# Performance work log

Measured on AMD Instinct MI355X. Metric: run time of the kernel, lower is better.

## Reference

```python
import jax, jax.numpy as jnp
import numpy as np

N_NODES = 50000
N_EDGES = 600000
D = 128


def setup_inputs() -> dict:
    key = jax.random.key(0)
    ks = jax.random.split(key, 8)
    s = 0.05
    return {
        "x": jax.random.normal(ks[0], (N_NODES, D), jnp.float32),
        "edge_index": jax.random.randint(ks[1], (2, N_EDGES), 0, N_NODES, jnp.int64),
        "edge_attr": jax.random.normal(ks[2], (N_EDGES, D), jnp.float32),
        "We1": jax.random.normal(ks[3], (3 * D, D), jnp.float32) * s,
        "be1": jnp.zeros((D,), jnp.float32),
        "We2": jax.random.normal(ks[4], (D, D), jnp.float32) * s,
        "be2": jnp.zeros((D,), jnp.float32),
        "Wn1": jax.random.normal(ks[5], (2 * D, D), jnp.float32) * s,
        "bn1": jnp.zeros((D,), jnp.float32),
        "Wn2": jax.random.normal(ks[6], (D, D), jnp.float32) * s,
        "bn2": jnp.zeros((D,), jnp.float32),
    }


def reference(x, edge_index, edge_attr, We1, be1, We2, be2, Wn1, bn1, Wn2, bn2):
    src = edge_index[0]
    dest = edge_index[1]
    n = x.shape[0]
    # edge model: MLP on [x_src | x_dest | edge_attr]  -> [E, D]
    e_in = jnp.concatenate([x[src], x[dest], edge_attr], axis=-1)
    e = jax.nn.relu(e_in @ We1 + be1) @ We2 + be2
    # node model: scatter-mean of updated edge_attr into dest nodes
    agg = jax.ops.segment_sum(e, dest, num_segments=n)
    cnt = jax.ops.segment_sum(jnp.ones((e.shape[0],), e.dtype), dest, num_segments=n)
    agg = agg / jnp.maximum(cnt, 1.0)[:, None]
    n_in = jnp.concatenate([x, agg], axis=-1)
    x_out = jax.nn.relu(n_in @ Wn1 + bn1) @ Wn2 + bn2
    return x_out, e
```

## Files before the change

kernel.cpp:

```cpp
#include <hip/hip_runtime.h>
#include <hip/hip_bf16.h>

#define DD 128

typedef short bf16x8 __attribute__((ext_vector_type(8)));
typedef float f32x4 __attribute__((ext_vector_type(4)));

__device__ __forceinline__ unsigned short f2b(float f) {
  unsigned int u = __float_as_uint(f);
  u = u + 0x7FFFu + ((u >> 16) & 1u);
  return (unsigned short)(u >> 16);
}

#define GLDS16(gp, lp) __builtin_amdgcn_global_load_lds( \
    (const __attribute__((address_space(1))) unsigned int*)(const void*)(gp), \
    (__attribute__((address_space(3))) unsigned int*)(void*)(lp), 16, 0, 0)

__global__ __launch_bounds__(256) void cvt_x_kernel(const float* __restrict__ x,
                                                    unsigned short* __restrict__ xb, int n4) {
  const int i = blockIdx.x * 256 + threadIdx.x;
  if (i < n4) {
    const float4 v = reinterpret_cast<const float4*>(x)[i];
    ushort4 o;
    o.x = f2b(v.x); o.y = f2b(v.y); o.z = f2b(v.z); o.w = f2b(v.w);
    reinterpret_cast<ushort4*>(xb)[i] = o;
  }
}

__global__ void count_kernel(const int* __restrict__ ei, int* __restrict__ cnt, int E) {
  int i = blockIdx.x * blockDim.x + threadIdx.x;
  if (i < E) atomicAdd(&cnt[ei[E + i]], 1);
}

__global__ __launch_bounds__(256) void scan_a(const int* __restrict__ cnt,
                                              int* __restrict__ off,
                                              int* __restrict__ bsum, int N) {
  __shared__ int wsum[4];
  const int t = threadIdx.x;
  const int i0 = blockIdx.x * 1024 + t * 4;
  int4 v = {0, 0, 0, 0};
  if (i0 + 3 < N) v = *reinterpret_cast<const int4*>(cnt + i0);
  else {
    if (i0 < N)     v.x = cnt[i0];
    if (i0 + 1 < N) v.y = cnt[i0 + 1];
    if (i0 + 2 < N) v.z = cnt[i0 + 2];
    if (i0 + 3 < N) v.w = cnt[i0 + 3];
  }
  const int s1 = v.x, s2 = s1 + v.y, s3 = s2 + v.z, tot = s3 + v.w;
  const int lane = t & 63, wv = t >> 6;
  int sc = tot;
#pragma unroll
  for (int d = 1; d < 64; d <<= 1) {
    int u = __shfl_up(sc, d);
    if (lane >= d) sc += u;
  }
  if (lane == 63) wsum[wv] = sc;
  __syncthreads();
  int wpre = 0;
  for (int w = 0; w < wv; ++w) wpre += wsum[w];
  const int excl = wpre + sc - tot;
  if (i0 < N)     off[i0]     = excl;
  if (i0 + 1 < N) off[i0 + 1] = excl + s1;
  if (i0 + 2 < N) off[i0 + 2] = excl + s2;
  if (i0 + 3 < N) off[i0 + 3] = excl + s3;
  if (t == 255) bsum[blockIdx.x] = wpre + sc;
}

__global__ void scan_b(int* __restrict__ bsum, int B) {
  const int t = threadIdx.x;
  const int v0 = (t < B) ? bsum[t] : 0;
  int v = v0;
#pragma unroll
  for (int d = 1; d < 64; d <<= 1) {
    int u = __shfl_up(v, d);
    if (t >= d) v += u;
  }
  if (t < B) bsum[t] = v - v0;
}

__global__ __launch_bounds__(256) void scan_c(int* __restrict__ off, int* __restrict__ cur,
                                              const int* __restrict__ bsum, int N, int E) {
  const int t = threadIdx.x;
  const int add = bsum[blockIdx.x];
  const int i0 = blockIdx.x * 1024 + t * 4;
#pragma unroll
  for (int k = 0; k < 4; ++k) {
    const int i = i0 + k;
    if (i < N) {
      const int o = off[i] + add;
      off[i] = o;
      cur[i] = o;
    }
  }
  if (blockIdx.x == 0 && t == 0) off[N] = E;
}

__global__ void fill_kernel(const int* __restrict__ ei, int* __restrict__ cur,
                            int* __restrict__ perm, int E) {
  int i = blockIdx.x * blockDim.x + threadIdx.x;
  if (i < E) {
    const int d = ei[E + i];
    const int pos = atomicAdd(&cur[d], 1);
    perm[pos] = i;
  }
}

__global__ __launch_bounds__(256, 2) void edge_mlp_kernel(
    const unsigned short* __restrict__ xb,
    const int* __restrict__ ei,
    const float* __restrict__ ea,
    const float* __restrict__ We1,
    const float* __restrict__ be1,
    const float* __restrict__ We2,
    const float* __restrict__ be2,
    float* __restrict__ e_out,
    int E)
{
  __shared__ __align__(16) unsigned short xs_lds[64][128];
  __shared__ __align__(16) unsigned short xd_lds[64][128];
  __shared__ __align__(16) unsigned short ea_lds[64][128];
  __shared__ __align__(16) unsigned short h_lds[64][136];
  __shared__ int srcs[64], dsts[64];

  const int tid  = threadIdx.x;
  const int wv   = tid >> 6;
  const int lane = tid & 63;
  const int lg   = lane >> 4;
  const int lm   = lane & 15;

  bf16x8 w1f[12][2];
  bf16x8 w2f[4][2];
  float b1[2], b2[2];
#pragma unroll
  for (int nf = 0; nf < 2; ++nf) {
    const int n = wv * 32 + nf * 16 + lm;
    b1[nf] = be1[n];
    b2[nf] = be2[n];
#pragma unroll
    for (int kb = 0; kb < 12; ++kb) {
      bf16x8 f;
#pragma unroll
      for (int j = 0; j < 8; ++j)
        f[j] = (short)f2b(We1[(kb * 32 + lg * 8 + j) * DD + n]);
      w1f[kb][nf] = f;
    }
#pragma unroll
    for (int kb = 0; kb < 4; ++kb) {
      bf16x8 f;
#pragma unroll
      for (int j = 0; j < 8; ++j)
        f[j] = (short)f2b(We2[(kb * 32 + lg * 8 + j) * DD + n]);
      w2f[kb][nf] = f;
    }
  }

  const int ntiles = E >> 6;
  for (int tile = blockIdx.x; tile < ntiles; tile += gridDim.x) {
    const int ebase = tile << 6;
    __syncthreads();

    if (tid < 64)       srcs[tid]      = ei[ebase + tid];
    else if (tid < 128) dsts[tid - 64] = ei[E + ebase + tid - 64];
    __syncthreads();

    {
#pragma unroll
      for (int wl = 0; wl < 4; ++wl) {
        const int r0 = wv * 16 + wl * 4;
        const int r  = r0 + (lane >> 4);
        const int ch = (lane & 15) ^ (r & 7);
        GLDS16(xb + (size_t)srcs[r] * DD + ch * 8, &xs_lds[r0][0]);
        GLDS16(xb + (size_t)dsts[r] * DD + ch * 8, &xd_lds[r0][0]);
      }
    }

    {
      float4 va[4], vb[4];
#pragma unroll
      for (int it = 0; it < 4; ++it) {
        const int q = tid + it * 256;
        const int r = q >> 4;
        const int c = q & 15;
        const float* p = ea + (size_t)(ebase + r) * DD + c * 8;
        va[it] = *reinterpret_cast<const float4*>(p);
        vb[it] = *reinterpret_cast<const float4*>(p + 4);
      }
#pragma unroll
      for (int it = 0; it < 4; ++it) {
        const int q = tid + it * 256;
        const int r = q >> 4;
        const int c = q & 15;
        bf16x8 o;
        o[0] = (short)f2b(va[it].x); o[1] = (short)f2b(va[it].y);
        o[2] = (short)f2b(va[it].z); o[3] = (short)f2b(va[it].w);
        o[4] = (short)f2b(vb[it].x); o[5] = (short)f2b(vb[it].y);
        o[6] = (short)f2b(vb[it].z); o[7] = (short)f2b(vb[it].w);
        *reinterpret_cast<bf16x8*>(&ea_lds[r][(c ^ (r & 7)) * 8]) = o;
      }
    }
    __syncthreads();

    f32x4 acc[4][2];
#pragma unroll
    for (int mf = 0; mf < 4; ++mf)
#pragma unroll
      for (int nf = 0; nf < 2; ++nf)
        acc[mf][nf] = (f32x4){0.f, 0.f, 0.f, 0.f};

#pragma unroll
    for (int kb = 0; kb < 12; ++kb) {
      const unsigned short (*blk)[128] = (kb < 4) ? xs_lds : (kb < 8) ? xd_lds : ea_lds;
      const int kl = kb & 3;
      bf16x8 a[4];
#pragma unroll
      for (int mf = 0; mf < 4; ++mf) {
        const int r = mf * 16 + lm;
        a[mf] = *reinterpret_cast<const bf16x8*>(&blk[r][((kl * 4 + lg) ^ (r & 7)) * 8]);
      }
#pragma unroll
      for (int mf = 0; mf < 4; ++mf)
#pragma unroll
        for (int nf = 0; nf < 2; ++nf)
          acc[mf][nf] = __builtin_amdgcn_mfma_f32_16x16x32_bf16(a[mf], w1f[kb][nf], acc[mf][nf], 0, 0, 0);
    }

#pragma unroll
    for (int mf = 0; mf < 4; ++mf)
#pragma unroll
      for (int nf = 0; nf < 2; ++nf)
#pragma unroll
        for (int rg = 0; rg < 4; ++rg) {
          const int m = mf * 16 + lg * 4 + rg;
          const int n = wv * 32 + nf * 16 + lm;
          float v = acc[mf][nf][rg] + b1[nf];
          h_lds[m][n] = f2b(v > 0.f ? v : 0.f);
        }
    __syncthreads();

    f32x4 acc2[4][2];
#pragma unroll
    for (int mf = 0; mf < 4; ++mf)
#pragma unroll
      for (int nf = 0; nf < 2; ++nf)
        acc2[mf][nf] = (f32x4){0.f, 0.f, 0.f, 0.f};

#pragma unroll
    for (int kb = 0; kb < 4; ++kb) {
      bf16x8 a[4];
#pragma unroll
      for (int mf = 0; mf < 4; ++mf)
        a[mf] = *reinterpret_cast<const bf16x8*>(&h_lds[mf * 16 + lm][kb * 32 + lg * 8]);
#pragma unroll
      for (int mf = 0; mf < 4; ++mf)
#pragma unroll
        for (int nf = 0; nf < 2; ++nf)
          acc2[mf][nf] = __builtin_amdgcn_mfma_f32_16x16x32_bf16(a[mf], w2f[kb][nf], acc2[mf][nf], 0, 0, 0);
    }

#pragma unroll
    for (int mf = 0; mf < 4; ++mf)
#pragma unroll
      for (int rg = 0; rg < 4; ++rg) {
        const int gm = ebase + mf * 16 + lg * 4 + rg;
#pragma unroll
        for (int nf = 0; nf < 2; ++nf) {
          const int n = wv * 32 + nf * 16 + lm;
          e_out[(size_t)gm * DD + n] = acc2[mf][nf][rg] + b2[nf];
        }
      }
  }
}

__global__ __launch_bounds__(256) void agg_kernel(const float* __restrict__ e_out,
                                                  const int* __restrict__ off,
                                                  const int* __restrict__ perm,
                                                  float* __restrict__ agg, int N) {
  const int wv   = threadIdx.x >> 6;
  const int lane = threadIdx.x & 63;
  const int nid  = blockIdx.x * 4 + wv;
  if (nid >= N) return;
  const int o0 = off[nid], o1 = off[nid + 1];
  float2 s0 = {0.f, 0.f}, s1 = {0.f, 0.f}, s2 = {0.f, 0.f}, s3 = {0.f, 0.f};
  int j = o0;
  for (; j + 4 <= o1; j += 4) {
    const int r0 = perm[j], r1 = perm[j + 1], r2 = perm[j + 2], r3 = perm[j + 3];
    const float2 v0 = *reinterpret_cast<const float2*>(e_out + (size_t)r0 * DD + (lane << 1));
    const float2 v1 = *reinterpret_cast<const float2*>(e_out + (size_t)r1 * DD + (lane << 1));
    const float2 v2 = *reinterpret_cast<const float2*>(e_out + (size_t)r2 * DD + (lane << 1));
    const float2 v3 = *reinterpret_cast<const float2*>(e_out + (size_t)r3 * DD + (lane << 1));
    s0.x += v0.x; s0.y += v0.y;
    s1.x += v1.x; s1.y += v1.y;
    s2.x += v2.x; s2.y += v2.y;
    s3.x += v3.x; s3.y += v3.y;
  }
  for (; j < o1; ++j) {
    const int r = perm[j];
    const float2 v = *reinterpret_cast<const float2*>(e_out + (size_t)r * DD + (lane << 1));
    s0.x += v.x; s0.y += v.y;
  }
  const int deg = o1 - o0;
  const float inv = deg > 0 ? 1.f / (float)deg : 0.f;
  float2 o;
  o.x = (s0.x + s1.x + s2.x + s3.x) * inv;
  o.y = (s0.y + s1.y + s2.y + s3.y) * inv;
  *reinterpret_cast<float2*>(agg + (size_t)nid * DD + (lane << 1)) = o;
}

__global__ __launch_bounds__(256, 2) void node_mlp_kernel(
    const float* __restrict__ x,
    const float* __restrict__ Wn1,
    const float* __restrict__ bn1,
    const float* __restrict__ Wn2,
    const float* __restrict__ bn2,
    float* __restrict__ xout,
    int N)
{
  __shared__ __align__(16) unsigned short A_lds[64][264];
  __shared__ __align__(16) unsigned short h_lds[64][136];

  const int tid  = threadIdx.x;
  const int wv   = tid >> 6;
  const int lane = tid & 63;
  const int lg   = lane >> 4;
  const int lm   = lane & 15;

  bf16x8 w1f[8][2];
  bf16x8 w2f[4][2];
  float b1[2], b2[2];
#pragma unroll
  for (int nf = 0; nf < 2; ++nf) {
    const int n = wv * 32 + nf * 16 + lm;
    b1[nf] = bn1[n];
    b2[nf] = bn2[n];
#pragma unroll
    for (int kb = 0; kb < 8; ++kb) {
      bf16x8 f;
#pragma unroll
      for (int j = 0; j < 8; ++j)
        f[j] = (short)f2b(Wn1[(kb * 32 + lg * 8 + j) * DD + n]);
      w1f[kb][nf] = f;
    }
#pragma unroll
    for (int kb = 0; kb < 4; ++kb) {
      bf16x8 f;
#pragma unroll
      for (int j = 0; j < 8; ++j)
        f[j] = (short)f2b(Wn2[(kb * 32 + lg * 8 + j) * DD + n]);
      w2f[kb][nf] = f;
    }
  }

  const int ntiles = (N + 63) >> 6;
  for (int tile = blockIdx.x; tile < ntiles; tile += gridDim.x) {
    const int nbase = tile << 6;
    __syncthreads();

#pragma unroll
    for (int it = 0; it < 16; ++it) {
      const int q = tid + it * 256;
      const int r = q >> 6;
      const int c = q & 63;
      int gr = nbase + r;
      if (gr >= N) gr = N - 1;
      float4 v;
      if (c < 32) v = *reinterpret_cast<const float4*>(x + (size_t)gr * DD + (c << 2));
      else        v = *reinterpret_cast<const float4*>(xout + (size_t)gr * DD + ((c - 32) << 2));
      unsigned short* dst = &A_lds[r][c << 2];
      dst[0] = f2b(v.x); dst[1] = f2b(v.y); dst[2] = f2b(v.z); dst[3] = f2b(v.w);
    }
    __syncthreads();

    f32x4 acc[4][2];
#pragma unroll
    for (int mf = 0; mf < 4; ++mf)
#pragma unroll
      for (int nf = 0; nf < 2; ++nf)
        acc[mf][nf] = (f32x4){0.f, 0.f, 0.f, 0.f};

#pragma unroll
    for (int kb = 0; kb < 8; ++kb) {
      bf16x8 a[4];
#pragma unroll
      for (int mf = 0; mf < 4; ++mf)
        a[mf] = *reinterpret_cast<const bf16x8*>(&A_lds[mf * 16 + lm][kb * 32 + lg * 8]);
#pragma unroll
      for (int mf = 0; mf < 4; ++mf)
#pragma unroll
        for (int nf = 0; nf < 2; ++nf)
          acc[mf][nf] = __builtin_amdgcn_mfma_f32_16x16x32_bf16(a[mf], w1f[kb][nf], acc[mf][nf], 0, 0, 0);
    }

#pragma unroll
    for (int mf = 0; mf < 4; ++mf)
#pragma unroll
      for (int nf = 0; nf < 2; ++nf)
#pragma unroll
        for (int rg = 0; rg < 4; ++rg) {
          const int m = mf * 16 + lg * 4 + rg;
          const int n = wv * 32 + nf * 16 + lm;
          float v = acc[mf][nf][rg] + b1[nf];
          h_lds[m][n] = f2b(v > 0.f ? v : 0.f);
        }
    __syncthreads();

    f32x4 acc2[4][2];
#pragma unroll
    for (int mf = 0; mf < 4; ++mf)
#pragma unroll
      for (int nf = 0; nf < 2; ++nf)
        acc2[mf][nf] = (f32x4){0.f, 0.f, 0.f, 0.f};

#pragma unroll
    for (int kb = 0; kb < 4; ++kb) {
      bf16x8 a[4];
#pragma unroll
      for (int mf = 0; mf < 4; ++mf)
        a[mf] = *reinterpret_cast<const bf16x8*>(&h_lds[mf * 16 + lm][kb * 32 + lg * 8]);
#pragma unroll
      for (int mf = 0; mf < 4; ++mf)
#pragma unroll
        for (int nf = 0; nf < 2; ++nf)
          acc2[mf][nf] = __builtin_amdgcn_mfma_f32_16x16x32_bf16(a[mf], w2f[kb][nf], acc2[mf][nf], 0, 0, 0);
    }

#pragma unroll
    for (int mf = 0; mf < 4; ++mf)
#pragma unroll
      for (int rg = 0; rg < 4; ++rg) {
        const int gm = nbase + mf * 16 + lg * 4 + rg;
        if (gm < N) {
#pragma unroll
          for (int nf = 0; nf < 2; ++nf) {
            const int n = wv * 32 + nf * 16 + lm;
            xout[(size_t)gm * DD + n] = acc2[mf][nf][rg] + b2[nf];
          }
        }
      }
  }
}

extern "C" void kernel_launch(void* const* d_in, const int* in_sizes, int n_in,
                              void* d_out, int out_size, void* d_ws, size_t ws_size,
                              hipStream_t stream) {
  const float* x   = (const float*)d_in[0];
  const int*   ei  = (const int*)d_in[1];
  const float* ea  = (const float*)d_in[2];
  const float* We1 = (const float*)d_in[3];
  const float* be1 = (const float*)d_in[4];
  const float* We2 = (const float*)d_in[5];
  const float* be2 = (const float*)d_in[6];
  const float* Wn1 = (const float*)d_in[7];
  const float* bn1 = (const float*)d_in[8];
  const float* Wn2 = (const float*)d_in[9];
  const float* bn2 = (const float*)d_in[10];

  const int N = in_sizes[0] / DD;
  const int E = in_sizes[2] / DD;

  float* out   = (float*)d_out;
  float* xout  = out;
  float* e_out = out + (size_t)N * DD;

  unsigned short* xb = (unsigned short*)xout;

  int* cnt  = (int*)d_ws;
  int* off  = cnt + N;
  int* cur  = off + N + 1;
  int* perm = cur + N;
  int* bsum = perm + E;

  const int SCAN_B = (N + 1023) / 1024;

  hipMemsetAsync(cnt, 0, (size_t)N * sizeof(int), stream);

  cvt_x_kernel<<<(N * DD / 4 + 255) / 256, 256, 0, stream>>>(x, xb, N * DD / 4);

  count_kernel<<<(E + 255) / 256, 256, 0, stream>>>(ei, cnt, E);
  scan_a<<<SCAN_B, 256, 0, stream>>>(cnt, off, bsum, N);
  scan_b<<<1, 64, 0, stream>>>(bsum, SCAN_B);
  scan_c<<<SCAN_B, 256, 0, stream>>>(off, cur, bsum, N, E);
  fill_kernel<<<(E + 255) / 256, 256, 0, stream>>>(ei, cur, perm, E);

  edge_mlp_kernel<<<2048, 256, 0, stream>>>(xb, ei, ea, We1, be1, We2, be2, e_out, E);

  agg_kernel<<<(N + 3) / 4, 256, 0, stream>>>(e_out, off, perm, xout, N);

  const int node_tiles = (N + 63) / 64;
  node_mlp_kernel<<<node_tiles, 256, 0, stream>>>(x, Wn1, bn1, Wn2, bn2, xout, N);
}
```

Baseline: 385.2 us.

## Fuse mean aggregation into node MLP and transpose MFMA operands for vector stores

Removes the separate agg kernel: node_mlp now gathers each node's incoming edge rows through the CSR perm and writes the bf16 mean directly into its LDS A tile, so the agg buffer no longer round-trips through global memory. Both MLP kernels swap the MFMA operand order so each lane holds four consecutive output columns. That allows float4 bias loads, float4 global stores and bf16x4 LDS writes. The hidden-layer buffer now reuses the edge-attr and A-tile LDS with XOR swizzling and an extra barrier, which cuts LDS use and raises the launch-bounds occupancy hint from 2 to 3. The risk is that the per-row serial gather inside node_mlp (16 rows per wave) may load-balance worse than the old one-wave-per-node agg kernel.

```diff
diff --git a/kernel.cpp b/kernel.cpp
--- a/kernel.cpp
+++ b/kernel.cpp
@@ -4,6 +4,7 @@
 #define DD 128
 
 typedef short bf16x8 __attribute__((ext_vector_type(8)));
+typedef short bf16x4 __attribute__((ext_vector_type(4)));
 typedef float f32x4 __attribute__((ext_vector_type(4)));
 
 __device__ __forceinline__ unsigned short f2b(float f) {
@@ -105,7 +106,7 @@
   }
 }
 
-__global__ __launch_bounds__(256, 2) void edge_mlp_kernel(
+__global__ __launch_bounds__(256, 3) void edge_mlp_kernel(
     const unsigned short* __restrict__ xb,
     const int* __restrict__ ei,
     const float* __restrict__ ea,
@@ -118,8 +119,7 @@
 {
   __shared__ __align__(16) unsigned short xs_lds[64][128];
   __shared__ __align__(16) unsigned short xd_lds[64][128];
-  __shared__ __align__(16) unsigned short ea_lds[64][128];
-  __shared__ __align__(16) unsigned short h_lds[64][136];
+  __shared__ __align__(16) unsigned short u_lds[64][128];
   __shared__ int srcs[64], dsts[64];
 
   const int tid  = threadIdx.x;
@@ -130,12 +130,12 @@
 
   bf16x8 w1f[12][2];
   bf16x8 w2f[4][2];
-  float b1[2], b2[2];
+  float4 b1v[2], b2v[2];
 #pragma unroll
   for (int nf = 0; nf < 2; ++nf) {
     const int n = wv * 32 + nf * 16 + lm;
-    b1[nf] = be1[n];
-    b2[nf] = be2[n];
+    b1v[nf] = *reinterpret_cast<const float4*>(&be1[wv * 32 + nf * 16 + 4 * lg]);
+    b2v[nf] = *reinterpret_cast<const float4*>(&be2[wv * 32 + nf * 16 + 4 * lg]);
 #pragma unroll
     for (int kb = 0; kb < 12; ++kb) {
       bf16x8 f;
@@ -163,15 +163,13 @@
     else if (tid < 128) dsts[tid - 64] = ei[E + ebase + tid - 64];
     __syncthreads();
 
-    {
-#pragma unroll
-      for (int wl = 0; wl < 4; ++wl) {
-        const int r0 = wv * 16 + wl * 4;
-        const int r  = r0 + (lane >> 4);
-        const int ch = (lane & 15) ^ (r & 7);
-        GLDS16(xb + (size_t)srcs[r] * DD + ch * 8, &xs_lds[r0][0]);
-        GLDS16(xb + (size_t)dsts[r] * DD + ch * 8, &xd_lds[r0][0]);
-      }
+#pragma unroll
+    for (int wl = 0; wl < 4; ++wl) {
+      const int r0 = wv * 16 + wl * 4;
+      const int r  = r0 + lg;
+      const int ch = lm ^ (r & 7);
+      GLDS16(xb + (size_t)srcs[r] * DD + ch * 8, &xs_lds[r0][0]);
+      GLDS16(xb + (size_t)dsts[r] * DD + ch * 8, &xd_lds[r0][0]);
     }
 
     {
@@ -179,9 +177,7 @@
 #pragma unroll
       for (int it = 0; it < 4; ++it) {
         const int q = tid + it * 256;
-        const int r = q >> 4;
-        const int c = q & 15;
-        const float* p = ea + (size_t)(ebase + r) * DD + c * 8;
+        const float* p = ea + (size_t)(ebase + (q >> 4)) * DD + (q & 15) * 8;
         va[it] = *reinterpret_cast<const float4*>(p);
         vb[it] = *reinterpret_cast<const float4*>(p + 4);
       }
@@ -195,7 +191,7 @@
         o[2] = (short)f2b(va[it].z); o[3] = (short)f2b(va[it].w);
         o[4] = (short)f2b(vb[it].x); o[5] = (short)f2b(vb[it].y);
         o[6] = (short)f2b(vb[it].z); o[7] = (short)f2b(vb[it].w);
-        *reinterpret_cast<bf16x8*>(&ea_lds[r][(c ^ (r & 7)) * 8]) = o;
+        *reinterpret_cast<bf16x8*>(&u_lds[r][(c ^ (r & 7)) * 8]) = o;
       }
     }
     __syncthreads();
@@ -209,7 +205,7 @@
 
 #pragma unroll
     for (int kb = 0; kb < 12; ++kb) {
-      const unsigned short (*blk)[128] = (kb < 4) ? xs_lds : (kb < 8) ? xd_lds : ea_lds;
+      const unsigned short (*blk)[128] = (kb < 4) ? xs_lds : (kb < 8) ? xd_lds : u_lds;
       const int kl = kb & 3;
       bf16x8 a[4];
 #pragma unroll
@@ -221,20 +217,26 @@
       for (int mf = 0; mf < 4; ++mf)
 #pragma unroll
         for (int nf = 0; nf < 2; ++nf)
-          acc[mf][nf] = __builtin_amdgcn_mfma_f32_16x16x32_bf16(a[mf], w1f[kb][nf], acc[mf][nf], 0, 0, 0);
-    }
-
-#pragma unroll
-    for (int mf = 0; mf < 4; ++mf)
-#pragma unroll
-      for (int nf = 0; nf < 2; ++nf)
+          acc[mf][nf] = __builtin_amdgcn_mfma_f32_16x16x32_bf16(w1f[kb][nf], a[mf], acc[mf][nf], 0, 0, 0);
+    }
+    __syncthreads();
+
+#pragma unroll
+    for (int mf = 0; mf < 4; ++mf) {
+      const int m = mf * 16 + lm;
+#pragma unroll
+      for (int nf = 0; nf < 2; ++nf) {
+        bf16x4 hv;
 #pragma unroll
         for (int rg = 0; rg < 4; ++rg) {
-          const int m = mf * 16 + lg * 4 + rg;
-          const int n = wv * 32 + nf * 16 + lm;
-          float v = acc[mf][nf][rg] + b1[nf];
-          h_lds[m][n] = f2b(v > 0.f ? v : 0.f);
+          float v = acc[mf][nf][rg] +
+                    (rg == 0 ? b1v[nf].x : rg == 1 ? b1v[nf].y : rg == 2 ? b1v[nf].z : b1v[nf].w);
+          hv[rg] = (short)f2b(v > 0.f ? v : 0.f);
         }
+        const int ch = (wv * 4 + nf * 2 + (lg >> 1)) ^ (m & 7);
+        *reinterpret_cast<bf16x4*>(&u_lds[m][ch * 8 + 4 * (lg & 1)]) = hv;
+      }
+    }
     __syncthreads();
 
     f32x4 acc2[4][2];
@@ -248,66 +250,38 @@
     for (int kb = 0; kb < 4; ++kb) {
       bf16x8 a[4];
 #pragma unroll
+      for (int mf = 0; mf < 4; ++mf) {
+        const int r = mf * 16 + lm;
+        a[mf] = *reinterpret_cast<const bf16x8*>(&u_lds[r][((kb * 4 + lg) ^ (r & 7)) * 8]);
+      }
+#pragma unroll
       for (int mf = 0; mf < 4; ++mf)
-        a[mf] = *reinterpret_cast<const bf16x8*>(&h_lds[mf * 16 + lm][kb * 32 + lg * 8]);
-#pragma unroll
-      for (int mf = 0; mf < 4; ++mf)
 #pragma unroll
         for (int nf = 0; nf < 2; ++nf)
-          acc2[mf][nf] = __builtin_amdgcn_mfma_f32_16x16x32_bf16(a[mf], w2f[kb][nf], acc2[mf][nf], 0, 0, 0);
-    }
-
-#pragma unroll
-    for (int mf = 0; mf < 4; ++mf)
-#pragma unroll
-      for (int rg = 0; rg < 4; ++rg) {
-        const int gm = ebase + mf * 16 + lg * 4 + rg;
-#pragma unroll
-        for (int nf = 0; nf < 2; ++nf) {
-          const int n = wv * 32 + nf * 16 + lm;
-          e_out[(size_t)gm * DD + n] = acc2[mf][nf][rg] + b2[nf];
-        }
-      }
-  }
-}
-
-__global__ __launch_bounds__(256) void agg_kernel(const float* __restrict__ e_out,
-                                                  const int* __restrict__ off,
-                                                  const int* __restrict__ perm,
-                                                  float* __restrict__ agg, int N) {
-  const int wv   = threadIdx.x >> 6;
-  const int lane = threadIdx.x & 63;
-  const int nid  = blockIdx.x * 4 + wv;
-  if (nid >= N) return;
-  const int o0 = off[nid], o1 = off[nid + 1];
-  float2 s0 = {0.f, 0.f}, s1 = {0.f, 0.f}, s2 = {0.f, 0.f}, s3 = {0.f, 0.f};
-  int j = o0;
-  for (; j + 4 <= o1; j += 4) {
-    const int r0 = perm[j], r1 = perm[j + 1], r2 = perm[j + 2], r3 = perm[j + 3];
-    const float2 v0 = *reinterpret_cast<const float2*>(e_out + (size_t)r0 * DD + (lane << 1));
-    const float2 v1 = *reinterpret_cast<const float2*>(e_out + (size_t)r1 * DD + (lane << 1));
-    const float2 v2 = *reinterpret_cast<const float2*>(e_out + (size_t)r2 * DD + (lane << 1));
-    const float2 v3 = *reinterpret_cast<const float2*>(e_out + (size_t)r3 * DD + (lane << 1));
-    s0.x += v0.x; s0.y += v0.y;
-    s1.x += v1.x; s1.y += v1.y;
-    s2.x += v2.x; s2.y += v2.y;
-    s3.x += v3.x; s3.y += v3.y;
-  }
-  for (; j < o1; ++j) {
-    const int r = perm[j];
-    const float2 v = *reinterpret_cast<const float2*>(e_out + (size_t)r * DD + (lane << 1));
-    s0.x += v.x; s0.y += v.y;
-  }
-  const int deg = o1 - o0;
-  const float inv = deg > 0 ? 1.f / (float)deg : 0.f;
-  float2 o;
-  o.x = (s0.x + s1.x + s2.x + s3.x) * inv;
-  o.y = (s0.y + s1.y + s2.y + s3.y) * inv;
-  *reinterpret_cast<float2*>(agg + (size_t)nid * DD + (lane << 1)) = o;
-}
-
-__global__ __launch_bounds__(256, 2) void node_mlp_kernel(
+          acc2[mf][nf] = __builtin_amdgcn_mfma_f32_16x16x32_bf16(w2f[kb][nf], a[mf], acc2[mf][nf], 0, 0, 0);
+    }
+
+#pragma unroll
+    for (int mf = 0; mf < 4; ++mf) {
+      const int gm = ebase + mf * 16 + lm;
+#pragma unroll
+      for (int nf = 0; nf < 2; ++nf) {
+        float4 o;
+        o.x = acc2[mf][nf][0] + b2v[nf].x;
+        o.y = acc2[mf][nf][1] + b2v[nf].y;
+        o.z = acc2[mf][nf][2] + b2v[nf].z;
+        o.w = acc2[mf][nf][3] + b2v[nf].w;
+        *reinterpret_cast<float4*>(&e_out[(size_t)gm * DD + wv * 32 + nf * 16 + 4 * lg]) = o;
+      }
+    }
+  }
+}
+
+__global__ __launch_bounds__(256, 3) void node_mlp_kernel(
     const float* __restrict__ x,
+    const float* __restrict__ e_out,
+    const int* __restrict__ off,
+    const int* __restrict__ perm,
     const float* __restrict__ Wn1,
     const float* __restrict__ bn1,
     const float* __restrict__ Wn2,
@@ -315,8 +289,7 @@
     float* __restrict__ xout,
     int N)
 {
-  __shared__ __align__(16) unsigned short A_lds[64][264];
-  __shared__ __align__(16) unsigned short h_lds[64][136];
+  __shared__ __align__(16) unsigned short A_lds[64 * 256];
 
   const int tid  = threadIdx.x;
   const int wv   = tid >> 6;
@@ -326,12 +299,12 @@
 
   bf16x8 w1f[8][2];
   bf16x8 w2f[4][2];
-  float b1[2], b2[2];
+  float4 b1v[2], b2v[2];
 #pragma unroll
   for (int nf = 0; nf < 2; ++nf) {
     const int n = wv * 32 + nf * 16 + lm;
-    b1[nf] = bn1[n];
-    b2[nf] = bn2[n];
+    b1v[nf] = *reinterpret_cast<const float4*>(&bn1[wv * 32 + nf * 16 + 4 * lg]);
+    b2v[nf] = *reinterpret_cast<const float4*>(&bn2[wv * 32 + nf * 16 + 4 * lg]);
 #pragma unroll
     for (int kb = 0; kb < 8; ++kb) {
       bf16x8 f;
@@ -356,17 +329,47 @@
     __syncthreads();
 
 #pragma unroll
-    for (int it = 0; it < 16; ++it) {
+    for (int it = 0; it < 4; ++it) {
       const int q = tid + it * 256;
-      const int r = q >> 6;
-      const int c = q & 63;
-      int gr = nbase + r;
-      if (gr >= N) gr = N - 1;
-      float4 v;
-      if (c < 32) v = *reinterpret_cast<const float4*>(x + (size_t)gr * DD + (c << 2));
-      else        v = *reinterpret_cast<const float4*>(xout + (size_t)gr * DD + ((c - 32) << 2));
-      unsigned short* dst = &A_lds[r][c << 2];
-      dst[0] = f2b(v.x); dst[1] = f2b(v.y); dst[2] = f2b(v.z); dst[3] = f2b(v.w);
+      const int r = q >> 4;
+      const int c = q & 15;
+      int gr = nbase + r; if (gr >= N) gr = N - 1;
+      const float* p = x + (size_t)gr * DD + c * 8;
+      const float4 va = *reinterpret_cast<const float4*>(p);
+      const float4 vb = *reinterpret_cast<const float4*>(p + 4);
+      bf16x8 o;
+      o[0] = (short)f2b(va.x); o[1] = (short)f2b(va.y);
+      o[2] = (short)f2b(va.z); o[3] = (short)f2b(va.w);
+      o[4] = (short)f2b(vb.x); o[5] = (short)f2b(vb.y);
+      o[6] = (short)f2b(vb.z); o[7] = (short)f2b(vb.w);
+      *reinterpret_cast<bf16x8*>(&A_lds[r * 256 + ((c ^ (r & 7)) * 8)]) = o;
+    }
+
+    for (int rr = 0; rr < 16; ++rr) {
+      const int row = wv * 16 + rr;
+      int gr = nbase + row; if (gr >= N) gr = N - 1;
+      const int o0 = off[gr], o1 = off[gr + 1];
+      float sx0 = 0.f, sy0 = 0.f, sx1 = 0.f, sy1 = 0.f;
+      int j = o0;
+      for (; j + 2 <= o1; j += 2) {
+        const int p0 = perm[j], p1 = perm[j + 1];
+        const float2 v0 = *reinterpret_cast<const float2*>(e_out + (size_t)p0 * DD + 2 * lane);
+        const float2 v1 = *reinterpret_cast<const float2*>(e_out + (size_t)p1 * DD + 2 * lane);
+        sx0 += v0.x; sy0 += v0.y;
+        sx1 += v1.x; sy1 += v1.y;
+      }
+      if (j < o1) {
+        const int p0 = perm[j];
+        const float2 v0 = *reinterpret_cast<const float2*>(e_out + (size_t)p0 * DD + 2 * lane);
+        sx0 += v0.x; sy0 += v0.y;
+      }
+      const int deg = o1 - o0;
+      const float inv = deg > 0 ? 1.f / (float)deg : 0.f;
+      const unsigned int pk = (unsigned int)f2b((sx0 + sx1) * inv) |
+                              ((unsigned int)f2b((sy0 + sy1) * inv) << 16);
+      const int cA = 16 + (lane >> 2);
+      *reinterpret_cast<unsigned int*>(
+          &A_lds[row * 256 + ((cA ^ (row & 7)) * 8) + 2 * (lane & 3)]) = pk;
     }
     __syncthreads();
 
@@ -381,26 +384,35 @@
     for (int kb = 0; kb < 8; ++kb) {
       bf16x8 a[4];
 #pragma unroll
+      for (int mf = 0; mf < 4; ++mf) {
+        const int r = mf * 16 + lm;
+        a[mf] = *reinterpret_cast<const bf16x8*>(
+            &A_lds[r * 256 + (((kb * 4 + lg) ^ (r & 7)) * 8)]);
+      }
+#pragma unroll
       for (int mf = 0; mf < 4; ++mf)
-        a[mf] = *reinterpret_cast<const bf16x8*>(&A_lds[mf * 16 + lm][kb * 32 + lg * 8]);
-#pragma unroll
-      for (int mf = 0; mf < 4; ++mf)
 #pragma unroll
         for (int nf = 0; nf < 2; ++nf)
-          acc[mf][nf] = __builtin_amdgcn_mfma_f32_16x16x32_bf16(a[mf], w1f[kb][nf], acc[mf][nf], 0, 0, 0);
-    }
-
-#pragma unroll
-    for (int mf = 0; mf < 4; ++mf)
-#pragma unroll
-      for (int nf = 0; nf < 2; ++nf)
+          acc[mf][nf] = __builtin_amdgcn_mfma_f32_16x16x32_bf16(w1f[kb][nf], a[mf], acc[mf][nf], 0, 0, 0);
+    }
+    __syncthreads();
+
+#pragma unroll
+    for (int mf = 0; mf < 4; ++mf) {
+      const int m = mf * 16 + lm;
+#pragma unroll
+      for (int nf = 0; nf < 2; ++nf) {
+        bf16x4 hv;
 #pragma unroll
         for (int rg = 0; rg < 4; ++rg) {
-          const int m = mf * 16 + lg * 4 + rg;
-          const int n = wv * 32 + nf * 16 + lm;
-          float v = acc[mf][nf][rg] + b1[nf];
-          h_lds[m][n] = f2b(v > 0.f ? v : 0.f);
+          float v = acc[mf][nf][rg] +
+                    (rg == 0 ? b1v[nf].x : rg == 1 ? b1v[nf].y : rg == 2 ? b1v[nf].z : b1v[nf].w);
+          hv[rg] = (short)f2b(v > 0.f ? v : 0.f);
         }
+        const int ch = (wv * 4 + nf * 2 + (lg >> 1)) ^ (m & 7);
+        *reinterpret_cast<bf16x4*>(&A_lds[m * 128 + ch * 8 + 4 * (lg & 1)]) = hv;
+      }
+    }
     __syncthreads();
 
     f32x4 acc2[4][2];
@@ -414,28 +426,33 @@
     for (int kb = 0; kb < 4; ++kb) {
       bf16x8 a[4];
 #pragma unroll
+      for (int mf = 0; mf < 4; ++mf) {
+        const int r = mf * 16 + lm;
+        a[mf] = *reinterpret_cast<const bf16x8*>(
+            &A_lds[r * 128 + (((kb * 4 + lg) ^ (r & 7)) * 8)]);
+      }
+#pragma unroll
       for (int mf = 0; mf < 4; ++mf)
-        a[mf] = *reinterpret_cast<const bf16x8*>(&h_lds[mf * 16 + lm][kb * 32 + lg * 8]);
-#pragma unroll
-      for (int mf = 0; mf < 4; ++mf)
 #pragma unroll
         for (int nf = 0; nf < 2; ++nf)
-          acc2[mf][nf] = __builtin_amdgcn_mfma_f32_16x16x32_bf16(a[mf], w2f[kb][nf], acc2[mf][nf], 0, 0, 0);
-    }
-
-#pragma unroll
-    for (int mf = 0; mf < 4; ++mf)
-#pragma unroll
-      for (int rg = 0; rg < 4; ++rg) {
-        const int gm = nbase + mf * 16 + lg * 4 + rg;
-        if (gm < N) {
-#pragma unroll
-          for (int nf = 0; nf < 2; ++nf) {
-            const int n = wv * 32 + nf * 16 + lm;
-            xout[(size_t)gm * DD + n] = acc2[mf][nf][rg] + b2[nf];
-          }
+          acc2[mf][nf] = __builtin_amdgcn_mfma_f32_16x16x32_bf16(w2f[kb][nf], a[mf], acc2[mf][nf], 0, 0, 0);
+    }
+
+#pragma unroll
+    for (int mf = 0; mf < 4; ++mf) {
+      const int gm = nbase + mf * 16 + lm;
+      if (gm < N) {
+#pragma unroll
+        for (int nf = 0; nf < 2; ++nf) {
+          float4 o;
+          o.x = acc2[mf][nf][0] + b2v[nf].x;
+          o.y = acc2[mf][nf][1] + b2v[nf].y;
+          o.z = acc2[mf][nf][2] + b2v[nf].z;
+          o.w = acc2[mf][nf][3] + b2v[nf].w;
+          *reinterpret_cast<float4*>(&xout[(size_t)gm * DD + wv * 32 + nf * 16 + 4 * lg]) = o;
         }
       }
+    }
   }
 }
 
@@ -483,8 +500,7 @@
 
   edge_mlp_kernel<<<2048, 256, 0, stream>>>(xb, ei, ea, We1, be1, We2, be2, e_out, E);
 
-  agg_kernel<<<(N + 3) / 4, 256, 0, stream>>>(e_out, off, perm, xout, N);
-
   const int node_tiles = (N + 63) / 64;
-  node_mlp_kernel<<<node_tiles, 256, 0, stream>>>(x, Wn1, bn1, Wn2, bn2, xout, N);
-}
+  node_mlp_kernel<<<node_tiles, 256, 0, stream>>>(x, e_out, off, perm,
+                                                  Wn1, bn1, Wn2, bn2, xout, N);
+}
```

Result: slower. 619.8 us (+60.9%).

## Precompute per-node src/dest projections of We1 and gather them per edge

Applied to the files above, without the earlier changes.

Splits the first edge-layer GEMM by linearity: a new kernel computes x@We1[0:128] and x@We1[128:256] once per node into a bf16 buffer. The edge kernel then gathers these per-edge projections as the accumulator initialisation and only runs the edge_attr third of the K dimension. This removes two thirds of the edge-layer MFMA work and the gathered x tiles from LDS, which lowers LDS use and allows higher occupancy. In exchange, the per-edge gather becomes scalar bf16 loads of 256-wide rows, and the projections are rounded to bf16 before summation.

```diff
diff --git a/kernel.cpp b/kernel.cpp
--- a/kernel.cpp
+++ b/kernel.cpp
@@ -11,20 +11,8 @@
   u = u + 0x7FFFu + ((u >> 16) & 1u);
   return (unsigned short)(u >> 16);
 }
-
-#define GLDS16(gp, lp) __builtin_amdgcn_global_load_lds( \
-    (const __attribute__((address_space(1))) unsigned int*)(const void*)(gp), \
-    (__attribute__((address_space(3))) unsigned int*)(void*)(lp), 16, 0, 0)
-
-__global__ __launch_bounds__(256) void cvt_x_kernel(const float* __restrict__ x,
-                                                    unsigned short* __restrict__ xb, int n4) {
-  const int i = blockIdx.x * 256 + threadIdx.x;
-  if (i < n4) {
-    const float4 v = reinterpret_cast<const float4*>(x)[i];
-    ushort4 o;
-    o.x = f2b(v.x); o.y = f2b(v.y); o.z = f2b(v.z); o.w = f2b(v.w);
-    reinterpret_cast<ushort4*>(xb)[i] = o;
-  }
+__device__ __forceinline__ float b2f(unsigned short u) {
+  return __uint_as_float((unsigned int)u << 16);
 }
 
 __global__ void count_kernel(const int* __restrict__ ei, int* __restrict__ cnt, int E) {
@@ -105,8 +93,93 @@
   }
 }
 
-__global__ __launch_bounds__(256, 2) void edge_mlp_kernel(
-    const unsigned short* __restrict__ xb,
+__global__ __launch_bounds__(256, 2) void pq_kernel(
+    const float* __restrict__ x,
+    const float* __restrict__ We1,
+    unsigned short* __restrict__ pq,
+    int N)
+{
+  __shared__ __align__(16) unsigned short x_lds[64][128];
+
+  const int tid  = threadIdx.x;
+  const int wv   = tid >> 6;
+  const int lane = tid & 63;
+  const int lg   = lane >> 4;
+  const int lm   = lane & 15;
+
+  bf16x8 wf[4][4];
+#pragma unroll
+  for (int nf = 0; nf < 4; ++nf) {
+    const int n    = wv * 64 + nf * 16 + lm;
+    const int col  = n & 127;
+    const int kro  = (n >> 7) * 128;
+#pragma unroll
+    for (int kb = 0; kb < 4; ++kb) {
+      bf16x8 f;
+#pragma unroll
+      for (int j = 0; j < 8; ++j)
+        f[j] = (short)f2b(We1[(kro + kb * 32 + lg * 8 + j) * DD + col]);
+      wf[kb][nf] = f;
+    }
+  }
+
+  const int nbase = blockIdx.x * 64;
+
+#pragma unroll
+  for (int it = 0; it < 4; ++it) {
+    const int q = tid + it * 256;
+    const int r = q >> 4;
+    const int c = q & 15;
+    int gr = nbase + r; if (gr >= N) gr = N - 1;
+    const float* p = x + (size_t)gr * DD + c * 8;
+    const float4 va = *reinterpret_cast<const float4*>(p);
+    const float4 vb = *reinterpret_cast<const float4*>(p + 4);
+    bf16x8 o;
+    o[0] = (short)f2b(va.x); o[1] = (short)f2b(va.y);
+    o[2] = (short)f2b(va.z); o[3] = (short)f2b(va.w);
+    o[4] = (short)f2b(vb.x); o[5] = (short)f2b(vb.y);
+    o[6] = (short)f2b(vb.z); o[7] = (short)f2b(vb.w);
+    *reinterpret_cast<bf16x8*>(&x_lds[r][(c ^ (r & 7)) * 8]) = o;
+  }
+  __syncthreads();
+
+  f32x4 acc[4][4];
+#pragma unroll
+  for (int mf = 0; mf < 4; ++mf)
+#pragma unroll
+    for (int nf = 0; nf < 4; ++nf)
+      acc[mf][nf] = (f32x4){0.f, 0.f, 0.f, 0.f};
+
+#pragma unroll
+  for (int kb = 0; kb < 4; ++kb) {
+    bf16x8 a[4];
+#pragma unroll
+    for (int mf = 0; mf < 4; ++mf) {
+      const int r = mf * 16 + lm;
+      a[mf] = *reinterpret_cast<const bf16x8*>(&x_lds[r][((kb * 4 + lg) ^ (r & 7)) * 8]);
+    }
+#pragma unroll
+    for (int mf = 0; mf < 4; ++mf)
+#pragma unroll
+      for (int nf = 0; nf < 4; ++nf)
+        acc[mf][nf] = __builtin_amdgcn_mfma_f32_16x16x32_bf16(a[mf], wf[kb][nf], acc[mf][nf], 0, 0, 0);
+  }
+
+#pragma unroll
+  for (int mf = 0; mf < 4; ++mf)
+#pragma unroll
+    for (int rg = 0; rg < 4; ++rg) {
+      const int gm = nbase + mf * 16 + lg * 4 + rg;
+      if (gm < N) {
+#pragma unroll
+        for (int nf = 0; nf < 4; ++nf)
+          pq[(size_t)gm * 256 + wv * 64 + nf * 16 + lm] = f2b(acc[mf][nf][rg]);
+      }
+    }
+}
+
+__global__ __launch_bounds__(256, 3) void edge_mlp_kernel(
+    const unsigned short* __restrict__ pq,
     const int* __restrict__ ei,
     const float* __restrict__ ea,
     const float* __restrict__ We1,
@@ -116,8 +189,6 @@
     float* __restrict__ e_out,
     int E)
 {
-  __shared__ __align__(16) unsigned short xs_lds[64][128];
-  __shared__ __align__(16) unsigned short xd_lds[64][128];
   __shared__ __align__(16) unsigned short ea_lds[64][128];
   __shared__ __align__(16) unsigned short h_lds[64][136];
   __shared__ int srcs[64], dsts[64];
@@ -128,7 +199,7 @@
   const int lg   = lane >> 4;
   const int lm   = lane & 15;
 
-  bf16x8 w1f[12][2];
+  bf16x8 w1f[4][2];
   bf16x8 w2f[4][2];
   float b1[2], b2[2];
 #pragma unroll
@@ -137,11 +208,11 @@
     b1[nf] = be1[n];
     b2[nf] = be2[n];
 #pragma unroll
-    for (int kb = 0; kb < 12; ++kb) {
+    for (int kb = 0; kb < 4; ++kb) {
       bf16x8 f;
 #pragma unroll
       for (int j = 0; j < 8; ++j)
-        f[j] = (short)f2b(We1[(kb * 32 + lg * 8 + j) * DD + n]);
+        f[j] = (short)f2b(We1[(256 + kb * 32 + lg * 8 + j) * DD + n]);
       w1f[kb][nf] = f;
     }
 #pragma unroll
@@ -163,59 +234,51 @@
     else if (tid < 128) dsts[tid - 64] = ei[E + ebase + tid - 64];
     __syncthreads();
 
-    {
-#pragma unroll
-      for (int wl = 0; wl < 4; ++wl) {
-        const int r0 = wv * 16 + wl * 4;
-        const int r  = r0 + (lane >> 4);
-        const int ch = (lane & 15) ^ (r & 7);
-        GLDS16(xb + (size_t)srcs[r] * DD + ch * 8, &xs_lds[r0][0]);
-        GLDS16(xb + (size_t)dsts[r] * DD + ch * 8, &xd_lds[r0][0]);
+    float4 va[4], vb[4];
+#pragma unroll
+    for (int it = 0; it < 4; ++it) {
+      const int q = tid + it * 256;
+      const float* p = ea + (size_t)(ebase + (q >> 4)) * DD + (q & 15) * 8;
+      va[it] = *reinterpret_cast<const float4*>(p);
+      vb[it] = *reinterpret_cast<const float4*>(p + 4);
+    }
+
+    f32x4 acc[4][2];
+#pragma unroll
+    for (int mf = 0; mf < 4; ++mf)
+#pragma unroll
+      for (int rg = 0; rg < 4; ++rg) {
+        const int m = mf * 16 + lg * 4 + rg;
+        const size_t rs = (size_t)srcs[m] * 256;
+        const size_t rd = (size_t)dsts[m] * 256;
+#pragma unroll
+        for (int nf = 0; nf < 2; ++nf) {
+          const int n = wv * 32 + nf * 16 + lm;
+          acc[mf][nf][rg] = b2f(pq[rs + n]) + b2f(pq[rd + 128 + n]);
+        }
       }
-    }
-
-    {
-      float4 va[4], vb[4];
-#pragma unroll
-      for (int it = 0; it < 4; ++it) {
-        const int q = tid + it * 256;
-        const int r = q >> 4;
-        const int c = q & 15;
-        const float* p = ea + (size_t)(ebase + r) * DD + c * 8;
-        va[it] = *reinterpret_cast<const float4*>(p);
-        vb[it] = *reinterpret_cast<const float4*>(p + 4);
-      }
-#pragma unroll
-      for (int it = 0; it < 4; ++it) {
-        const int q = tid + it * 256;
-        const int r = q >> 4;
-        const int c = q & 15;
-        bf16x8 o;
-        o[0] = (short)f2b(va[it].x); o[1] = (short)f2b(va[it].y);
-        o[2] = (short)f2b(va[it].z); o[3] = (short)f2b(va[it].w);
-        o[4] = (short)f2b(vb[it].x); o[5] = (short)f2b(vb[it].y);
-        o[6] = (short)f2b(vb[it].z); o[7] = (short)f2b(vb[it].w);
-        *reinterpret_cast<bf16x8*>(&ea_lds[r][(c ^ (r & 7)) * 8]) = o;
-      }
-    }
-    __syncthreads();
-
-    f32x4 acc[4][2];
-#pragma unroll
-    for (int mf = 0; mf < 4; ++mf)
-#pragma unroll
-      for (int nf = 0; nf < 2; ++nf)
-        acc[mf][nf] = (f32x4){0.f, 0.f, 0.f, 0.f};
-
-#pragma unroll
-    for (int kb = 0; kb < 12; ++kb) {
-      const unsigned short (*blk)[128] = (kb < 4) ? xs_lds : (kb < 8) ? xd_lds : ea_lds;
-      const int kl = kb & 3;
+
+#pragma unroll
+    for (int it = 0; it < 4; ++it) {
+      const int q = tid + it * 256;
+      const int r = q >> 4;
+      const int c = q & 15;
+      bf16x8 o;
+      o[0] = (short)f2b(va[it].x); o[1] = (short)f2b(va[it].y);
+      o[2] = (short)f2b(va[it].z); o[3] = (short)f2b(va[it].w);
+      o[4] = (short)f2b(vb[it].x); o[5] = (short)f2b(vb[it].y);
+      o[6] = (short)f2b(vb[it].z); o[7] = (short)f2b(vb[it].w);
+      *reinterpret_cast<bf16x8*>(&ea_lds[r][(c ^ (r & 7)) * 8]) = o;
+    }
+    __syncthreads();
+
+#pragma unroll
+    for (int kb = 0; kb < 4; ++kb) {
       bf16x8 a[4];
 #pragma unroll
       for (int mf = 0; mf < 4; ++mf) {
         const int r = mf * 16 + lm;
-        a[mf] = *reinterpret_cast<const bf16x8*>(&blk[r][((kl * 4 + lg) ^ (r & 7)) * 8]);
+        a[mf] = *reinterpret_cast<const bf16x8*>(&ea_lds[r][((kb * 4 + lg) ^ (r & 7)) * 8]);
       }
 #pragma unroll
       for (int mf = 0; mf < 4; ++mf)
@@ -461,7 +524,7 @@
   float* xout  = out;
   float* e_out = out + (size_t)N * DD;
 
-  unsigned short* xb = (unsigned short*)xout;
+  unsigned short* pq = (unsigned short*)xout;
 
   int* cnt  = (int*)d_ws;
   int* off  = cnt + N;
@@ -473,7 +536,7 @@
 
   hipMemsetAsync(cnt, 0, (size_t)N * sizeof(int), stream);
 
-  cvt_x_kernel<<<(N * DD / 4 + 255) / 256, 256, 0, stream>>>(x, xb, N * DD / 4);
+  pq_kernel<<<(N + 63) / 64, 256, 0, stream>>>(x, We1, pq, N);
 
   count_kernel<<<(E + 255) / 256, 256, 0, stream>>>(ei, cnt, E);
   scan_a<<<SCAN_B, 256, 0, stream>>>(cnt, off, bsum, N);
@@ -481,7 +544,7 @@
   scan_c<<<SCAN_B, 256, 0, stream>>>(off, cur, bsum, N, E);
   fill_kernel<<<(E + 255) / 256, 256, 0, stream>>>(ei, cur, perm, E);
 
-  edge_mlp_kernel<<<2048, 256, 0, stream>>>(xb, ei, ea, We1, be1, We2, be2, e_out, E);
+  edge_mlp_kernel<<<2048, 256, 0, stream>>>(pq, ei, ea, We1, be1, We2, be2, e_out, E);
 
   agg_kernel<<<(N + 3) / 4, 256, 0, stream>>>(e_out, off, perm, xout, N);
 
```

After: 401.5 us. 1.04x slower.
